# Kernel optimization log

Hardware: AMD Instinct MI355X
Metric: run time of the kernel (lower is better)

Reference implementation:

```python
import jax, jax.numpy as jnp
import numpy as np
import math

B, L, H, E = 16, 1024, 8, 64   # L = nsensor = N (forced by einsum 'bhls,bhlg')
WIN = 1024                      # win_size, last dim of x
G = 64                          # n_group
D_SEL = 1                       # d_sel default


def setup_inputs() -> dict:
    key = jax.random.key(0)
    ks = jax.random.split(key, 7)
    return {
        "queries": jax.random.normal(ks[0], (B, L, H, E), dtype=jnp.float32),
        "keys": jax.random.normal(ks[1], (B, L, H, E), dtype=jnp.float32),
        "values": jax.random.normal(ks[2], (B, L, H, E), dtype=jnp.float32),
        "x": jax.random.normal(ks[3], (B, L, WIN), dtype=jnp.float32),
        "mlp_w": jax.random.normal(ks[4], (H * D_SEL, WIN), dtype=jnp.float32) * 0.02,
        "mlp_b": jax.random.normal(ks[5], (H * D_SEL,), dtype=jnp.float32) * 0.02,
        "sel_W": jax.random.normal(ks[6], (H, G, D_SEL), dtype=jnp.float32),
        "attn_mask": 0,
    }


def _select_attention(x, mlp_w, mlp_b, sel_W, n_heads, d_sel):
    b, n, lwin = x.shape
    xf = x.reshape(b * n, lwin)
    newx = jnp.tanh(xf @ mlp_w.T + mlp_b)                 # [(B*N), H*d_sel]
    # Faithful raw reshape (torch.reshape, no permute): mixes n and h axes.
    newx = newx.reshape(b, n_heads, n, d_sel)             # [B, H, N, d_sel]
    sel = jnp.einsum('bhnd,hgd->bhng', newx, sel_W)       # [B, H, N, G]
    return jax.nn.relu(sel)


def reference(queries, keys, values, x, mlp_w, mlp_b, sel_W, attn_mask):
    b, l, h, e = queries.shape
    scale = 1.0 / math.sqrt(e)
    scores = jnp.einsum('blhe,bshe->bhls', queries, keys)      # [B, H, L, S]
    sel = _select_attention(x, mlp_w, mlp_b, sel_W, h, D_SEL)  # [B, H, L, G]
    scores = jnp.einsum('bhls,bhlg->bhsg', scores, sel)        # [B, H, S, G]
    series = jax.nn.softmax(scale * scores, axis=-1)           # softmax over groups
    # values labeled 'blhs': l=S (value len), s=D (feature). Output V: [B, D, H, G]
    V = jnp.einsum('blhs,bhlg->bshg', values, series)
    return V
```

## Files before the change

### kernel.cpp

```cpp
#include <hip/hip_runtime.h>
#include <math.h>

#define NB 16
#define NL 1024
#define NH 8
#define NE 64
#define NWIN 1024
#define NG 64

#define SCH 128
#define SROW 136

typedef __attribute__((ext_vector_type(8))) short short8;
typedef __attribute__((ext_vector_type(4))) float floatx4;

__device__ __forceinline__ short f2bf(float x) {
    unsigned u = __float_as_uint(x);
    u += 0x7fffu + ((u >> 16) & 1u);
    return (short)(u >> 16);
}
__device__ __forceinline__ float dot4(float4 a, float4 b) {
    return fmaf(a.x, b.x, fmaf(a.y, b.y, fmaf(a.z, b.z, a.w * b.w)));
}
__device__ __forceinline__ void lgkm_barrier() {
    asm volatile("s_waitcnt lgkmcnt(0)" ::: "memory");
    __builtin_amdgcn_s_barrier();
}
__device__ __forceinline__ void lgkm_wait() {
    asm volatile("s_waitcnt lgkmcnt(0)" ::: "memory");
}

__global__ __launch_bounds__(256, 4) void k_sel_q(
    const float* __restrict__ x, const float* __restrict__ mlp_w,
    const float* __restrict__ mlp_b, const float* __restrict__ q,
    float* __restrict__ qp, float* __restrict__ qn)
{
    __shared__ float4 w_lds[8][NWIN / 4];
    __shared__ float t_lds[128];
    __shared__ float redp[4][64], redn[4][64];

    int tid = threadIdx.x;
    int blk = blockIdx.x;
    int ee = blk & 7, bh = blk >> 3;
    int b = bh >> 3, h = bh & 7;
    int w = tid >> 6, lane = tid & 63;
    int sq = lane >> 4, c = lane & 15;

    const float4* w4 = (const float4*)mlp_w;
    float4* wl = (float4*)w_lds;
    #pragma unroll
    for (int i = 0; i < 8; ++i)
        wl[tid + 256 * i] = w4[tid + 256 * i];
    __syncthreads();

    int row_loc = w * 4 + sq;
    int r = b * 1024 + h * 128 + ee * 16 + row_loc;
    const float4* xr = (const float4*)(x + (size_t)r * NWIN);
    float4 a03 = make_float4(0,0,0,0), a47 = make_float4(0,0,0,0);
    #pragma unroll
    for (int i = 0; i < 16; ++i) {
        float4 xv = xr[i * 16 + c];
        a03.x += dot4(xv, w_lds[0][i * 16 + c]);
        a03.y += dot4(xv, w_lds[1][i * 16 + c]);
        a03.z += dot4(xv, w_lds[2][i * 16 + c]);
        a03.w += dot4(xv, w_lds[3][i * 16 + c]);
        a47.x += dot4(xv, w_lds[4][i * 16 + c]);
        a47.y += dot4(xv, w_lds[5][i * 16 + c]);
        a47.z += dot4(xv, w_lds[6][i * 16 + c]);
        a47.w += dot4(xv, w_lds[7][i * 16 + c]);
    }
    #pragma unroll
    for (int off = 1; off < 16; off <<= 1) {
        a03.x += __shfl_xor(a03.x, off, 64);
        a03.y += __shfl_xor(a03.y, off, 64);
        a03.z += __shfl_xor(a03.z, off, 64);
        a03.w += __shfl_xor(a03.w, off, 64);
        a47.x += __shfl_xor(a47.x, off, 64);
        a47.y += __shfl_xor(a47.y, off, 64);
        a47.z += __shfl_xor(a47.z, off, 64);
        a47.w += __shfl_xor(a47.w, off, 64);
    }
    if (c == 0) {
        float4 b03 = *(const float4*)mlp_b;
        float4 b47 = *(const float4*)(mlp_b + 4);
        float4 t03, t47;
        t03.x = tanhf(a03.x + b03.x); t03.y = tanhf(a03.y + b03.y);
        t03.z = tanhf(a03.z + b03.z); t03.w = tanhf(a03.w + b03.w);
        t47.x = tanhf(a47.x + b47.x); t47.y = tanhf(a47.y + b47.y);
        t47.z = tanhf(a47.z + b47.z); t47.w = tanhf(a47.w + b47.w);
        *(float4*)&t_lds[row_loc * 8]     = t03;
        *(float4*)&t_lds[row_loc * 8 + 4] = t47;
    }
    lgkm_wait();

    int lo = sq, e4 = c;
    float4 accp = make_float4(0,0,0,0), accn = make_float4(0,0,0,0);
    #pragma unroll
    for (int i = 0; i < 8; ++i) {
        int l_loc = w * 32 + i * 4 + lo;
        float tv = t_lds[l_loc];
        int l = ee * 128 + l_loc;
        float4 qv = *(const float4*)(q + (((size_t)(b * NL + l)) * NH + h) * NE + e4 * 4);
        float tp = fmaxf(tv, 0.f), tn = fminf(tv, 0.f);
        accp.x = fmaf(tp, qv.x, accp.x); accp.y = fmaf(tp, qv.y, accp.y);
        accp.z = fmaf(tp, qv.z, accp.z); accp.w = fmaf(tp, qv.w, accp.w);
        accn.x = fmaf(tn, qv.x, accn.x); accn.y = fmaf(tn, qv.y, accn.y);
        accn.z = fmaf(tn, qv.z, accn.z); accn.w = fmaf(tn, qv.w, accn.w);
    }
    #pragma unroll
    for (int off = 16; off <= 32; off <<= 1) {
        accp.x += __shfl_xor(accp.x, off, 64); accp.y += __shfl_xor(accp.y, off, 64);
        accp.z += __shfl_xor(accp.z, off, 64); accp.w += __shfl_xor(accp.w, off, 64);
        accn.x += __shfl_xor(accn.x, off, 64); accn.y += __shfl_xor(accn.y, off, 64);
        accn.z += __shfl_xor(accn.z, off, 64); accn.w += __shfl_xor(accn.w, off, 64);
    }
    if (lo == 0) {
        *(float4*)&redp[w][e4 * 4] = accp;
        *(float4*)&redn[w][e4 * 4] = accn;
    }
    __syncthreads();
    if (tid < 64) {
        atomicAdd(&qp[bh * NE + tid], redp[0][tid] + redp[1][tid] + redp[2][tid] + redp[3][tid]);
    } else if (tid < 128) {
        int e = tid - 64;
        atomicAdd(&qn[bh * NE + e], redn[0][e] + redn[1][e] + redn[2][e] + redn[3][e]);
    }
}

__global__ __launch_bounds__(256, 4) void k_attn_out(
    const float* __restrict__ keys, const float* __restrict__ values,
    const float* __restrict__ sel_W,
    const float* __restrict__ qp, const float* __restrict__ qn,
    float* __restrict__ out)
{
    __shared__ short sb[NG][SROW];
    __shared__ float ap_l[SCH], an_l[SCH];
    __shared__ float2 wpn[4][NG];

    int tid = threadIdx.x, blk = blockIdx.x;
    int chunk = blk & 7, bh = blk >> 3;
    int b = bh >> 3, h = bh & 7;
    int w = tid >> 6, lane = tid & 63;
    int c = lane & 15, sq = lane >> 4;
    const float scale = 0.125f;
    int s0 = chunk * SCH;

    {
        float W = sel_W[h * NG + lane];
        wpn[w][lane] = make_float2(fmaxf(W, 0.f) * scale, fminf(W, 0.f) * scale);
    }

    const float4 qp4 = *(const float4*)(qp + bh * NE + c * 4);
    const float4 qn4 = *(const float4*)(qn + bh * NE + c * 4);

    float4 kvv[8];
    #pragma unroll
    for (int p = 0; p < 8; ++p) {
        int sl = w * 32 + p * 4 + sq;
        kvv[p] = *(const float4*)(keys + (((size_t)(b * NL + s0 + sl)) * NH + h) * NE + c * 4);
    }
    const float* vbase = values + (((size_t)(b * NL + s0)) * NH + h) * NE + 16 * w + c;
    float vregA[16], vregB[16];
    #pragma unroll
    for (int m = 0; m < 16; ++m)
        vregA[m] = vbase[(size_t)((m >> 3) * 32 + sq * 8 + (m & 7)) * (NH * NE)];
    #pragma unroll
    for (int m = 0; m < 16; ++m)
        vregB[m] = vbase[(size_t)((2 + (m >> 3)) * 32 + sq * 8 + (m & 7)) * (NH * NE)];
    __builtin_amdgcn_sched_barrier(0);

    #pragma unroll
    for (int p = 0; p < 8; ++p) {
        int sl = w * 32 + p * 4 + sq;
        float pp = dot4(kvv[p], qp4);
        float pn = dot4(kvv[p], qn4);
        #pragma unroll
        for (int m_ = 1; m_ <= 8; m_ <<= 1) {
            pp += __shfl_xor(pp, m_, 64);
            pn += __shfl_xor(pn, m_, 64);
        }
        if (c == 0) { ap_l[sl] = pp; an_l[sl] = pn; }
    }
    lgkm_wait();

    {
        int s_ = w * 32 + (lane & 31);
        int g0 = (lane >> 5) * 32;
        float ap = ap_l[s_], an = an_l[s_];
        const float2* wv_ = &wpn[w][g0];
        float m = -1e30f;
        #pragma unroll 8
        for (int g = 0; g < 32; ++g) {
            float2 wv = wv_[g];
            m = fmaxf(m, fmaf(wv.x, ap, wv.y * an));
        }
        m = fmaxf(m, __shfl_xor(m, 32, 64));
        float d = 0.f;
        #pragma unroll 8
        for (int g = 0; g < 32; ++g) {
            float2 wv = wv_[g];
            d += __expf(fmaf(wv.x, ap, wv.y * an) - m);
        }
        d += __shfl_xor(d, 32, 64);
        float inv = 1.0f / d;
        #pragma unroll 8
        for (int g = 0; g < 32; ++g) {
            float2 wv = wv_[g];
            sb[g0 + g][s_] = f2bf(__expf(fmaf(wv.x, ap, wv.y * an) - m) * inv);
        }
    }
    lgkm_barrier();

    floatx4 acc[4] = {{0.f,0.f,0.f,0.f},{0.f,0.f,0.f,0.f},
                      {0.f,0.f,0.f,0.f},{0.f,0.f,0.f,0.f}};
    #pragma unroll
    for (int ks = 0; ks < 4; ++ks) {
        short8 av;
        #pragma unroll
        for (int j = 0; j < 8; ++j)
            av[j] = f2bf(ks < 2 ? vregA[ks * 8 + j] : vregB[(ks - 2) * 8 + j]);
        #pragma unroll
        for (int n = 0; n < 4; ++n) {
            short8 bv = *(const short8*)&sb[16 * n + c][ks * 32 + sq * 8];
            acc[n] = __builtin_amdgcn_mfma_f32_16x16x32_bf16(av, bv, acc[n], 0, 0, 0);
        }
    }

    #pragma unroll
    for (int n = 0; n < 4; ++n) {
        #pragma unroll
        for (int r = 0; r < 4; ++r) {
            int e = 16 * w + sq * 4 + r;
            int g = 16 * n + c;
            atomicAdd(&out[((size_t)(b * NE + e) * NH + h) * NG + g], acc[n][r]);
        }
    }
}

extern "C" void kernel_launch(void* const* d_in, const int* in_sizes, int n_in,
                              void* d_out, int out_size, void* d_ws, size_t ws_size,
                              hipStream_t stream) {
    (void)in_sizes; (void)n_in; (void)ws_size;
    const float* queries = (const float*)d_in[0];
    const float* keys    = (const float*)d_in[1];
    const float* values  = (const float*)d_in[2];
    const float* x       = (const float*)d_in[3];
    const float* mlp_w   = (const float*)d_in[4];
    const float* mlp_b   = (const float*)d_in[5];
    const float* sel_W   = (const float*)d_in[6];
    float* out = (float*)d_out;

    float* qp_ws = (float*)d_ws;
    float* qn_ws = qp_ws + NB * NH * NE;

    hipMemsetAsync(out, 0, (size_t)out_size * sizeof(float), stream);
    hipMemsetAsync(qp_ws, 0, (size_t)2 * NB * NH * NE * sizeof(float), stream);

    k_sel_q<<<dim3(NB * NH * 8), dim3(256), 0, stream>>>(x, mlp_w, mlp_b,
                                                          queries, qp_ws, qn_ws);
    k_attn_out<<<dim3(NB * NH * 8), dim3(256), 0, stream>>>(keys, values, sel_W,
                                                            qp_ws, qn_ws, out);
}
```

Baseline: 199.6 us.

## Process two x rows per thread group in k_sel_q and halve grid

After: 198.4 us. Within noise of the previous version (-0.6%).

```diff
diff --git a/kernel.cpp b/kernel.cpp
--- a/kernel.cpp
+++ b/kernel.cpp
@@ -30,21 +30,22 @@
     asm volatile("s_waitcnt lgkmcnt(0)" ::: "memory");
 }
 
-__global__ __launch_bounds__(256, 4) void k_sel_q(
+__global__ __launch_bounds__(256, 2) void k_sel_q(
     const float* __restrict__ x, const float* __restrict__ mlp_w,
     const float* __restrict__ mlp_b, const float* __restrict__ q,
     float* __restrict__ qp, float* __restrict__ qn)
 {
     __shared__ float4 w_lds[8][NWIN / 4];
-    __shared__ float t_lds[128];
+    __shared__ float t_lds[256];
     __shared__ float redp[4][64], redn[4][64];
 
     int tid = threadIdx.x;
     int blk = blockIdx.x;
-    int ee = blk & 7, bh = blk >> 3;
+    int qq = blk & 3, bh = blk >> 2;
     int b = bh >> 3, h = bh & 7;
     int w = tid >> 6, lane = tid & 63;
     int sq = lane >> 4, c = lane & 15;
+    int gi = tid >> 4;
 
     const float4* w4 = (const float4*)mlp_w;
     float4* wl = (float4*)w_lds;
@@ -53,53 +54,79 @@
         wl[tid + 256 * i] = w4[tid + 256 * i];
     __syncthreads();
 
-    int row_loc = w * 4 + sq;
-    int r = b * 1024 + h * 128 + ee * 16 + row_loc;
-    const float4* xr = (const float4*)(x + (size_t)r * NWIN);
+    int r0 = b * 1024 + h * 128 + qq * 32 + gi * 2;
+    const float4* xr0 = (const float4*)(x + (size_t)r0 * NWIN);
+    const float4* xr1 = (const float4*)(x + (size_t)(r0 + 1) * NWIN);
+    float4 xv0[16], xv1[16];
+    #pragma unroll
+    for (int i = 0; i < 16; ++i) xv0[i] = xr0[i * 16 + c];
+    #pragma unroll
+    for (int i = 0; i < 16; ++i) xv1[i] = xr1[i * 16 + c];
+    __builtin_amdgcn_sched_barrier(0);
+
     float4 a03 = make_float4(0,0,0,0), a47 = make_float4(0,0,0,0);
+    float4 d03 = make_float4(0,0,0,0), d47 = make_float4(0,0,0,0);
     #pragma unroll
     for (int i = 0; i < 16; ++i) {
-        float4 xv = xr[i * 16 + c];
-        a03.x += dot4(xv, w_lds[0][i * 16 + c]);
-        a03.y += dot4(xv, w_lds[1][i * 16 + c]);
-        a03.z += dot4(xv, w_lds[2][i * 16 + c]);
-        a03.w += dot4(xv, w_lds[3][i * 16 + c]);
-        a47.x += dot4(xv, w_lds[4][i * 16 + c]);
-        a47.y += dot4(xv, w_lds[5][i * 16 + c]);
-        a47.z += dot4(xv, w_lds[6][i * 16 + c]);
-        a47.w += dot4(xv, w_lds[7][i * 16 + c]);
+        float4 w0 = w_lds[0][i * 16 + c];
+        float4 w1 = w_lds[1][i * 16 + c];
+        float4 w2 = w_lds[2][i * 16 + c];
+        float4 w3 = w_lds[3][i * 16 + c];
+        float4 w5 = w_lds[4][i * 16 + c];
+        float4 w6 = w_lds[5][i * 16 + c];
+        float4 w7 = w_lds[6][i * 16 + c];
+        float4 w8 = w_lds[7][i * 16 + c];
+        float4 xa = xv0[i], xb = xv1[i];
+        a03.x += dot4(xa, w0); a03.y += dot4(xa, w1);
+        a03.z += dot4(xa, w2); a03.w += dot4(xa, w3);
+        a47.x += dot4(xa, w5); a47.y += dot4(xa, w6);
+        a47.z += dot4(xa, w7); a47.w += dot4(xa, w8);
+        d03.x += dot4(xb, w0); d03.y += dot4(xb, w1);
+        d03.z += dot4(xb, w2); d03.w += dot4(xb, w3);
+        d47.x += dot4(xb, w5); d47.y += dot4(xb, w6);
+        d47.z += dot4(xb, w7); d47.w += dot4(xb, w8);
     }
     #pragma unroll
     for (int off = 1; off < 16; off <<= 1) {
-        a03.x += __shfl_xor(a03.x, off, 64);
-        a03.y += __shfl_xor(a03.y, off, 64);
-        a03.z += __shfl_xor(a03.z, off, 64);
-        a03.w += __shfl_xor(a03.w, off, 64);
-        a47.x += __shfl_xor(a47.x, off, 64);
-        a47.y += __shfl_xor(a47.y, off, 64);
-        a47.z += __shfl_xor(a47.z, off, 64);
-        a47.w += __shfl_xor(a47.w, off, 64);
-    }
-    if (c == 0) {
+        a03.x += __shfl_xor(a03.x, off, 64); a03.y += __shfl_xor(a03.y, off, 64);
+        a03.z += __shfl_xor(a03.z, off, 64); a03.w += __shfl_xor(a03.w, off, 64);
+        a47.x += __shfl_xor(a47.x, off, 64); a47.y += __shfl_xor(a47.y, off, 64);
+        a47.z += __shfl_xor(a47.z, off, 64); a47.w += __shfl_xor(a47.w, off, 64);
+        d03.x += __shfl_xor(d03.x, off, 64); d03.y += __shfl_xor(d03.y, off, 64);
+        d03.z += __shfl_xor(d03.z, off, 64); d03.w += __shfl_xor(d03.w, off, 64);
+        d47.x += __shfl_xor(d47.x, off, 64); d47.y += __shfl_xor(d47.y, off, 64);
+        d47.z += __shfl_xor(d47.z, off, 64); d47.w += __shfl_xor(d47.w, off, 64);
+    }
+    {
         float4 b03 = *(const float4*)mlp_b;
         float4 b47 = *(const float4*)(mlp_b + 4);
-        float4 t03, t47;
-        t03.x = tanhf(a03.x + b03.x); t03.y = tanhf(a03.y + b03.y);
-        t03.z = tanhf(a03.z + b03.z); t03.w = tanhf(a03.w + b03.w);
-        t47.x = tanhf(a47.x + b47.x); t47.y = tanhf(a47.y + b47.y);
-        t47.z = tanhf(a47.z + b47.z); t47.w = tanhf(a47.w + b47.w);
-        *(float4*)&t_lds[row_loc * 8]     = t03;
-        *(float4*)&t_lds[row_loc * 8 + 4] = t47;
+        if (c == 0) {
+            float4 t03, t47;
+            t03.x = tanhf(a03.x + b03.x); t03.y = tanhf(a03.y + b03.y);
+            t03.z = tanhf(a03.z + b03.z); t03.w = tanhf(a03.w + b03.w);
+            t47.x = tanhf(a47.x + b47.x); t47.y = tanhf(a47.y + b47.y);
+            t47.z = tanhf(a47.z + b47.z); t47.w = tanhf(a47.w + b47.w);
+            *(float4*)&t_lds[(gi * 2) * 8]     = t03;
+            *(float4*)&t_lds[(gi * 2) * 8 + 4] = t47;
+        } else if (c == 1) {
+            float4 t03, t47;
+            t03.x = tanhf(d03.x + b03.x); t03.y = tanhf(d03.y + b03.y);
+            t03.z = tanhf(d03.z + b03.z); t03.w = tanhf(d03.w + b03.w);
+            t47.x = tanhf(d47.x + b47.x); t47.y = tanhf(d47.y + b47.y);
+            t47.z = tanhf(d47.z + b47.z); t47.w = tanhf(d47.w + b47.w);
+            *(float4*)&t_lds[(gi * 2 + 1) * 8]     = t03;
+            *(float4*)&t_lds[(gi * 2 + 1) * 8 + 4] = t47;
+        }
     }
     lgkm_wait();
 
     int lo = sq, e4 = c;
     float4 accp = make_float4(0,0,0,0), accn = make_float4(0,0,0,0);
     #pragma unroll
-    for (int i = 0; i < 8; ++i) {
-        int l_loc = w * 32 + i * 4 + lo;
+    for (int i = 0; i < 16; ++i) {
+        int l_loc = w * 64 + i * 4 + lo;
         float tv = t_lds[l_loc];
-        int l = ee * 128 + l_loc;
+        int l = qq * 256 + l_loc;
         float4 qv = *(const float4*)(q + (((size_t)(b * NL + l)) * NH + h) * NE + e4 * 4);
         float tp = fmaxf(tv, 0.f), tn = fminf(tv, 0.f);
         accp.x = fmaf(tp, qv.x, accp.x); accp.y = fmaf(tp, qv.y, accp.y);
@@ -256,7 +283,7 @@
     hipMemsetAsync(out, 0, (size_t)out_size * sizeof(float), stream);
     hipMemsetAsync(qp_ws, 0, (size_t)2 * NB * NH * NE * sizeof(float), stream);
 
-    k_sel_q<<<dim3(NB * NH * 8), dim3(256), 0, stream>>>(x, mlp_w, mlp_b,
+    k_sel_q<<<dim3(NB * NH * 4), dim3(256), 0, stream>>>(x, mlp_w, mlp_b,
                                                           queries, qp_ws, qn_ws);
     k_attn_out<<<dim3(NB * NH * 8), dim3(256), 0, stream>>>(keys, values, sel_W,
                                                             qp_ws, qn_ws, out);
```

## Fuse selection projection and attention output into a single 1024-thread kernel

Applied to the files above, without the earlier changes.

After: 210.0 us. 1.05x slower.

```diff
diff --git a/kernel.cpp b/kernel.cpp
--- a/kernel.cpp
+++ b/kernel.cpp
@@ -8,8 +8,8 @@
 #define NWIN 1024
 #define NG 64
 
-#define SCH 128
-#define SROW 136
+#define SHALF 512
+#define SROW 520
 
 typedef __attribute__((ext_vector_type(8))) short short8;
 typedef __attribute__((ext_vector_type(4))) float floatx4;
@@ -30,128 +30,107 @@
     asm volatile("s_waitcnt lgkmcnt(0)" ::: "memory");
 }
 
-__global__ __launch_bounds__(256, 4) void k_sel_q(
+#define RED16(v) { v.x += __shfl_xor(v.x, off, 64); v.y += __shfl_xor(v.y, off, 64); \
+                   v.z += __shfl_xor(v.z, off, 64); v.w += __shfl_xor(v.w, off, 64); }
+#define TWRITE(pa, pb, row) { \
+    float4 t03, t47; \
+    t03.x = tanhf(pa.x + b03.x); t03.y = tanhf(pa.y + b03.y); \
+    t03.z = tanhf(pa.z + b03.z); t03.w = tanhf(pa.w + b03.w); \
+    t47.x = tanhf(pb.x + b47.x); t47.y = tanhf(pb.y + b47.y); \
+    t47.z = tanhf(pb.z + b47.z); t47.w = tanhf(pb.w + b47.w); \
+    *(float4*)&t_lds[(row) * 8]     = t03; \
+    *(float4*)&t_lds[(row) * 8 + 4] = t47; }
+
+__global__ __launch_bounds__(1024, 4) void k_mega(
     const float* __restrict__ x, const float* __restrict__ mlp_w,
     const float* __restrict__ mlp_b, const float* __restrict__ q,
-    float* __restrict__ qp, float* __restrict__ qn)
+    const float* __restrict__ keys, const float* __restrict__ values,
+    const float* __restrict__ sel_W, float* __restrict__ out)
 {
-    __shared__ float4 w_lds[8][NWIN / 4];
-    __shared__ float t_lds[128];
-    __shared__ float redp[4][64], redn[4][64];
-
-    int tid = threadIdx.x;
-    int blk = blockIdx.x;
-    int ee = blk & 7, bh = blk >> 3;
+    __shared__ __align__(16) char smem[71680];
+    float4 (*w_lds)[256] = (float4(*)[256])smem;
+    float*  t_lds        = (float*)(smem + 32768);
+    float  (*redp)[64]   = (float(*)[64])(smem + 36864);
+    float  (*redn)[64]   = (float(*)[64])(smem + 40960);
+    short  (*sb)[SROW]   = (short(*)[SROW])smem;
+    float*  ap_l         = (float*)(smem + 66560);
+    float*  an_l         = (float*)(smem + 68608);
+    float2* wpn          = (float2*)(smem + 70656);
+    float*  qp_l         = (float*)(smem + 71168);
+    float*  qn_l         = (float*)(smem + 71424);
+
+    int tid = threadIdx.x, blk = blockIdx.x;
+    int shalf = blk & 1, bh = blk >> 1;
     int b = bh >> 3, h = bh & 7;
     int w = tid >> 6, lane = tid & 63;
     int sq = lane >> 4, c = lane & 15;
-
-    const float4* w4 = (const float4*)mlp_w;
-    float4* wl = (float4*)w_lds;
-    #pragma unroll
-    for (int i = 0; i < 8; ++i)
-        wl[tid + 256 * i] = w4[tid + 256 * i];
+    const float scale = 0.125f;
+    int s0 = shalf * SHALF;
+
+    {
+        const float4* w4 = (const float4*)mlp_w;
+        float4* wl = (float4*)smem;
+        wl[tid]        = w4[tid];
+        wl[tid + 1024] = w4[tid + 1024];
+    }
+    if (tid < NG) {
+        float W = sel_W[h * NG + tid];
+        wpn[tid] = make_float2(fmaxf(W, 0.f) * scale, fminf(W, 0.f) * scale);
+    }
     __syncthreads();
 
-    int row_loc = w * 4 + sq;
-    int r = b * 1024 + h * 128 + ee * 16 + row_loc;
-    const float4* xr = (const float4*)(x + (size_t)r * NWIN);
-    float4 a03 = make_float4(0,0,0,0), a47 = make_float4(0,0,0,0);
-    #pragma unroll
-    for (int i = 0; i < 16; ++i) {
-        float4 xv = xr[i * 16 + c];
-        a03.x += dot4(xv, w_lds[0][i * 16 + c]);
-        a03.y += dot4(xv, w_lds[1][i * 16 + c]);
-        a03.z += dot4(xv, w_lds[2][i * 16 + c]);
-        a03.w += dot4(xv, w_lds[3][i * 16 + c]);
-        a47.x += dot4(xv, w_lds[4][i * 16 + c]);
-        a47.y += dot4(xv, w_lds[5][i * 16 + c]);
-        a47.z += dot4(xv, w_lds[6][i * 16 + c]);
-        a47.w += dot4(xv, w_lds[7][i * 16 + c]);
-    }
-    #pragma unroll
-    for (int off = 1; off < 16; off <<= 1) {
-        a03.x += __shfl_xor(a03.x, off, 64);
-        a03.y += __shfl_xor(a03.y, off, 64);
-        a03.z += __shfl_xor(a03.z, off, 64);
-        a03.w += __shfl_xor(a03.w, off, 64);
-        a47.x += __shfl_xor(a47.x, off, 64);
-        a47.y += __shfl_xor(a47.y, off, 64);
-        a47.z += __shfl_xor(a47.z, off, 64);
-        a47.w += __shfl_xor(a47.w, off, 64);
-    }
-    if (c == 0) {
+    if (w < 8) {
+        int gi = tid >> 4;
+        int r0 = b * 1024 + h * 128 + gi * 4;
+        const float4* x0 = (const float4*)(x + (size_t)r0 * NWIN);
+        const float4* x1 = (const float4*)(x + (size_t)(r0 + 1) * NWIN);
+        const float4* x2 = (const float4*)(x + (size_t)(r0 + 2) * NWIN);
+        const float4* x3 = (const float4*)(x + (size_t)(r0 + 3) * NWIN);
+        float4 p0a = make_float4(0,0,0,0), p0b = make_float4(0,0,0,0);
+        float4 p1a = make_float4(0,0,0,0), p1b = make_float4(0,0,0,0);
+        float4 p2a = make_float4(0,0,0,0), p2b = make_float4(0,0,0,0);
+        float4 p3a = make_float4(0,0,0,0), p3b = make_float4(0,0,0,0);
+        #pragma unroll
+        for (int i = 0; i < 16; ++i) {
+            float4 w0 = w_lds[0][i * 16 + c];
+            float4 w1 = w_lds[1][i * 16 + c];
+            float4 w2 = w_lds[2][i * 16 + c];
+            float4 w3 = w_lds[3][i * 16 + c];
+            float4 w4 = w_lds[4][i * 16 + c];
+            float4 w5 = w_lds[5][i * 16 + c];
+            float4 w6 = w_lds[6][i * 16 + c];
+            float4 w7 = w_lds[7][i * 16 + c];
+            float4 xa = x0[i * 16 + c], xb = x1[i * 16 + c];
+            float4 xc = x2[i * 16 + c], xd = x3[i * 16 + c];
+            p0a.x += dot4(xa, w0); p0a.y += dot4(xa, w1);
+            p0a.z += dot4(xa, w2); p0a.w += dot4(xa, w3);
+            p0b.x += dot4(xa, w4); p0b.y += dot4(xa, w5);
+            p0b.z += dot4(xa, w6); p0b.w += dot4(xa, w7);
+            p1a.x += dot4(xb, w0); p1a.y += dot4(xb, w1);
+            p1a.z += dot4(xb, w2); p1a.w += dot4(xb, w3);
+            p1b.x += dot4(xb, w4); p1b.y += dot4(xb, w5);
+            p1b.z += dot4(xb, w6); p1b.w += dot4(xb, w7);
+            p2a.x += dot4(xc, w0); p2a.y += dot4(xc, w1);
+            p2a.z += dot4(xc, w2); p2a.w += dot4(xc, w3);
+            p2b.x += dot4(xc, w4); p2b.y += dot4(xc, w5);
+            p2b.z += dot4(xc, w6); p2b.w += dot4(xc, w7);
+            p3a.x += dot4(xd, w0); p3a.y += dot4(xd, w1);
+            p3a.z += dot4(xd, w2); p3a.w += dot4(xd, w3);
+            p3b.x += dot4(xd, w4); p3b.y += dot4(xd, w5);
+            p3b.z += dot4(xd, w6); p3b.w += dot4(xd, w7);
+        }
+        #pragma unroll
+        for (int off = 1; off < 16; off <<= 1) {
+            RED16(p0a) RED16(p0b) RED16(p1a) RED16(p1b)
+            RED16(p2a) RED16(p2b) RED16(p3a) RED16(p3b)
+        }
         float4 b03 = *(const float4*)mlp_b;
         float4 b47 = *(const float4*)(mlp_b + 4);
-        float4 t03, t47;
-        t03.x = tanhf(a03.x + b03.x); t03.y = tanhf(a03.y + b03.y);
-        t03.z = tanhf(a03.z + b03.z); t03.w = tanhf(a03.w + b03.w);
-        t47.x = tanhf(a47.x + b47.x); t47.y = tanhf(a47.y + b47.y);
-        t47.z = tanhf(a47.z + b47.z); t47.w = tanhf(a47.w + b47.w);
-        *(float4*)&t_lds[row_loc * 8]     = t03;
-        *(float4*)&t_lds[row_loc * 8 + 4] = t47;
-    }
-    lgkm_wait();
-
-    int lo = sq, e4 = c;
-    float4 accp = make_float4(0,0,0,0), accn = make_float4(0,0,0,0);
-    #pragma unroll
-    for (int i = 0; i < 8; ++i) {
-        int l_loc = w * 32 + i * 4 + lo;
-        float tv = t_lds[l_loc];
-        int l = ee * 128 + l_loc;
-        float4 qv = *(const float4*)(q + (((size_t)(b * NL + l)) * NH + h) * NE + e4 * 4);
-        float tp = fmaxf(tv, 0.f), tn = fminf(tv, 0.f);
-        accp.x = fmaf(tp, qv.x, accp.x); accp.y = fmaf(tp, qv.y, accp.y);
-        accp.z = fmaf(tp, qv.z, accp.z); accp.w = fmaf(tp, qv.w, accp.w);
-        accn.x = fmaf(tn, qv.x, accn.x); accn.y = fmaf(tn, qv.y, accn.y);
-        accn.z = fmaf(tn, qv.z, accn.z); accn.w = fmaf(tn, qv.w, accn.w);
-    }
-    #pragma unroll
-    for (int off = 16; off <= 32; off <<= 1) {
-        accp.x += __shfl_xor(accp.x, off, 64); accp.y += __shfl_xor(accp.y, off, 64);
-        accp.z += __shfl_xor(accp.z, off, 64); accp.w += __shfl_xor(accp.w, off, 64);
-        accn.x += __shfl_xor(accn.x, off, 64); accn.y += __shfl_xor(accn.y, off, 64);
-        accn.z += __shfl_xor(accn.z, off, 64); accn.w += __shfl_xor(accn.w, off, 64);
-    }
-    if (lo == 0) {
-        *(float4*)&redp[w][e4 * 4] = accp;
-        *(float4*)&redn[w][e4 * 4] = accn;
-    }
-    __syncthreads();
-    if (tid < 64) {
-        atomicAdd(&qp[bh * NE + tid], redp[0][tid] + redp[1][tid] + redp[2][tid] + redp[3][tid]);
-    } else if (tid < 128) {
-        int e = tid - 64;
-        atomicAdd(&qn[bh * NE + e], redn[0][e] + redn[1][e] + redn[2][e] + redn[3][e]);
-    }
-}
-
-__global__ __launch_bounds__(256, 4) void k_attn_out(
-    const float* __restrict__ keys, const float* __restrict__ values,
-    const float* __restrict__ sel_W,
-    const float* __restrict__ qp, const float* __restrict__ qn,
-    float* __restrict__ out)
-{
-    __shared__ short sb[NG][SROW];
-    __shared__ float ap_l[SCH], an_l[SCH];
-    __shared__ float2 wpn[4][NG];
-
-    int tid = threadIdx.x, blk = blockIdx.x;
-    int chunk = blk & 7, bh = blk >> 3;
-    int b = bh >> 3, h = bh & 7;
-    int w = tid >> 6, lane = tid & 63;
-    int c = lane & 15, sq = lane >> 4;
-    const float scale = 0.125f;
-    int s0 = chunk * SCH;
-
-    {
-        float W = sel_W[h * NG + lane];
-        wpn[w][lane] = make_float2(fmaxf(W, 0.f) * scale, fminf(W, 0.f) * scale);
-    }
-
-    const float4 qp4 = *(const float4*)(qp + bh * NE + c * 4);
-    const float4 qn4 = *(const float4*)(qn + bh * NE + c * 4);
+        if      (c == 0) TWRITE(p0a, p0b, gi * 4 + 0)
+        else if (c == 1) TWRITE(p1a, p1b, gi * 4 + 1)
+        else if (c == 2) TWRITE(p2a, p2b, gi * 4 + 2)
+        else if (c == 3) TWRITE(p3a, p3b, gi * 4 + 3)
+    }
 
     float4 kvv[8];
     #pragma unroll
@@ -159,7 +138,39 @@
         int sl = w * 32 + p * 4 + sq;
         kvv[p] = *(const float4*)(keys + (((size_t)(b * NL + s0 + sl)) * NH + h) * NE + c * 4);
     }
-    const float* vbase = values + (((size_t)(b * NL + s0)) * NH + h) * NE + 16 * w + c;
+    __builtin_amdgcn_sched_barrier(0);
+
+    lgkm_barrier();
+
+    {
+        int lo = sq, e4 = c;
+        float4 accp = make_float4(0,0,0,0), accn = make_float4(0,0,0,0);
+        #pragma unroll
+        for (int i = 0; i < 16; ++i) {
+            int l = w * 64 + i * 4 + lo;
+            float tv = t_lds[l];
+            float4 qv = *(const float4*)(q + (((size_t)(b * NL + l)) * NH + h) * NE + e4 * 4);
+            float tp = fmaxf(tv, 0.f), tn = fminf(tv, 0.f);
+            accp.x = fmaf(tp, qv.x, accp.x); accp.y = fmaf(tp, qv.y, accp.y);
+            accp.z = fmaf(tp, qv.z, accp.z); accp.w = fmaf(tp, qv.w, accp.w);
+            accn.x = fmaf(tn, qv.x, accn.x); accn.y = fmaf(tn, qv.y, accn.y);
+            accn.z = fmaf(tn, qv.z, accn.z); accn.w = fmaf(tn, qv.w, accn.w);
+        }
+        #pragma unroll
+        for (int off = 16; off <= 32; off <<= 1) {
+            accp.x += __shfl_xor(accp.x, off, 64); accp.y += __shfl_xor(accp.y, off, 64);
+            accp.z += __shfl_xor(accp.z, off, 64); accp.w += __shfl_xor(accp.w, off, 64);
+            accn.x += __shfl_xor(accn.x, off, 64); accn.y += __shfl_xor(accn.y, off, 64);
+            accn.z += __shfl_xor(accn.z, off, 64); accn.w += __shfl_xor(accn.w, off, 64);
+        }
+        if (lo == 0) {
+            *(float4*)&redp[w][e4 * 4] = accp;
+            *(float4*)&redn[w][e4 * 4] = accn;
+        }
+    }
+
+    int et = w & 3, q_ = w >> 2;
+    const float* vbase = values + (((size_t)(b * NL + s0 + q_ * 128)) * NH + h) * NE + 16 * et + c;
     float vregA[16], vregB[16];
     #pragma unroll
     for (int m = 0; m < 16; ++m)
@@ -168,6 +179,24 @@
     for (int m = 0; m < 16; ++m)
         vregB[m] = vbase[(size_t)((2 + (m >> 3)) * 32 + sq * 8 + (m & 7)) * (NH * NE)];
     __builtin_amdgcn_sched_barrier(0);
+
+    lgkm_barrier();
+    if (tid < 64) {
+        float s = 0.f;
+        #pragma unroll
+        for (int i = 0; i < 16; ++i) s += redp[i][tid];
+        qp_l[tid] = s;
+    } else if (tid < 128) {
+        int e = tid - 64;
+        float s = 0.f;
+        #pragma unroll
+        for (int i = 0; i < 16; ++i) s += redn[i][e];
+        qn_l[e] = s;
+    }
+    lgkm_barrier();
+
+    const float4 qp4 = *(const float4*)&qp_l[c * 4];
+    const float4 qn4 = *(const float4*)&qn_l[c * 4];
 
     #pragma unroll
     for (int p = 0; p < 8; ++p) {
@@ -187,7 +216,7 @@
         int s_ = w * 32 + (lane & 31);
         int g0 = (lane >> 5) * 32;
         float ap = ap_l[s_], an = an_l[s_];
-        const float2* wv_ = &wpn[w][g0];
+        const float2* wv_ = &wpn[g0];
         float m = -1e30f;
         #pragma unroll 8
         for (int g = 0; g < 32; ++g) {
@@ -221,7 +250,7 @@
             av[j] = f2bf(ks < 2 ? vregA[ks * 8 + j] : vregB[(ks - 2) * 8 + j]);
         #pragma unroll
         for (int n = 0; n < 4; ++n) {
-            short8 bv = *(const short8*)&sb[16 * n + c][ks * 32 + sq * 8];
+            short8 bv = *(const short8*)&sb[16 * n + c][q_ * 128 + ks * 32 + sq * 8];
             acc[n] = __builtin_amdgcn_mfma_f32_16x16x32_bf16(av, bv, acc[n], 0, 0, 0);
         }
     }
@@ -230,7 +259,7 @@
     for (int n = 0; n < 4; ++n) {
         #pragma unroll
         for (int r = 0; r < 4; ++r) {
-            int e = 16 * w + sq * 4 + r;
+            int e = 16 * et + sq * 4 + r;
             int g = 16 * n + c;
             atomicAdd(&out[((size_t)(b * NE + e) * NH + h) * NG + g], acc[n][r]);
         }
@@ -240,7 +269,7 @@
 extern "C" void kernel_launch(void* const* d_in, const int* in_sizes, int n_in,
                               void* d_out, int out_size, void* d_ws, size_t ws_size,
                               hipStream_t stream) {
-    (void)in_sizes; (void)n_in; (void)ws_size;
+    (void)in_sizes; (void)n_in; (void)d_ws; (void)ws_size;
     const float* queries = (const float*)d_in[0];
     const float* keys    = (const float*)d_in[1];
     const float* values  = (const float*)d_in[2];
@@ -250,14 +279,7 @@
     const float* sel_W   = (const float*)d_in[6];
     float* out = (float*)d_out;
 
-    float* qp_ws = (float*)d_ws;
-    float* qn_ws = qp_ws + NB * NH * NE;
-
     hipMemsetAsync(out, 0, (size_t)out_size * sizeof(float), stream);
-    hipMemsetAsync(qp_ws, 0, (size_t)2 * NB * NH * NE * sizeof(float), stream);
-
-    k_sel_q<<<dim3(NB * NH * 8), dim3(256), 0, stream>>>(x, mlp_w, mlp_b,
-                                                          queries, qp_ws, qn_ws);
-    k_attn_out<<<dim3(NB * NH * 8), dim3(256), 0, stream>>>(keys, values, sel_W,
-                                                            qp_ws, qn_ws, out);
-}
+    k_mega<<<dim3(NB * NH * 2), dim3(1024), 0, stream>>>(
+        x, mlp_w, mlp_b, queries, keys, values, sel_W, out);
+}
```
